# Performance work log

Hardware: AMD Instinct MI355X
Metric: run time of the kernel (lower is better)

Reference implementation:

```python
import jax, jax.numpy as jnp
import numpy as np

B, T, H, L = 64, 2048, 256, 16


def setup_inputs() -> dict:
    key = jax.random.key(0)
    ks = jax.random.split(key, 6)
    x = jax.random.normal(ks[0], (B, T, H), dtype=jnp.float32)
    tags = jax.random.randint(ks[1], (B, T), 0, L).astype(jnp.int32)
    mask = jnp.ones((B, T), dtype=bool)  # torchcrf requires mask[:,0] all on
    W = jax.random.normal(ks[2], (L, H), dtype=jnp.float32) * (1.0 / np.sqrt(H))
    b = jnp.zeros((L,), dtype=jnp.float32)
    # torchcrf initializes transitions ~ U(-0.1, 0.1)
    start_transitions = jax.random.uniform(ks[3], (L,), minval=-0.1, maxval=0.1)
    end_transitions = jax.random.uniform(ks[4], (L,), minval=-0.1, maxval=0.1)
    transitions = jax.random.uniform(ks[5], (L, L), minval=-0.1, maxval=0.1)
    return {"x": x, "W": W, "b": b,
            "start_transitions": start_transitions,
            "end_transitions": end_transitions,
            "transitions": transitions,
            "tags": tags, "mask": mask}


def reference(x, W, b, start_transitions, end_transitions, transitions, tags, mask):
    # Emitter: Linear(hidden_dim -> num_labels)
    emissions = jnp.einsum('bth,lh->btl', x, W) + b  # [B,T,L]
    maskf = mask.astype(emissions.dtype)             # [B,T]

    # ---- numerator: score of the gold tag path (vectorized, no scan) ----
    emit_gold = jnp.take_along_axis(emissions, tags[..., None].astype(jnp.int32), axis=2)[..., 0]  # [B,T]
    first_tags = tags[:, 0]
    score = start_transitions[first_tags] + emit_gold[:, 0]
    trans_gold = transitions[tags[:, :-1], tags[:, 1:]]  # [B,T-1]
    score = score + jnp.sum((trans_gold + emit_gold[:, 1:]) * maskf[:, 1:], axis=1)
    seq_ends = jnp.sum(mask.astype(jnp.int32), axis=1) - 1  # index of last valid step
    last_tags = jnp.take_along_axis(tags, seq_ends[:, None], axis=1)[:, 0]
    score = score + end_transitions[last_tags]

    # ---- denominator: forward algorithm (log partition) via lax.scan over time ----
    em_t = jnp.swapaxes(emissions, 0, 1)  # [T,B,L]
    mask_t = jnp.swapaxes(mask, 0, 1)     # [T,B]
    alpha0 = start_transitions[None, :] + em_t[0]  # [B,L]

    def step(alpha, inp):
        em, m = inp  # em: [B,L], m: [B]
        # logsumexp over previous label: alpha[b,i] + transitions[i,j] + em[b,j]
        nxt = jax.nn.logsumexp(alpha[:, :, None] + transitions[None, :, :] + em[:, None, :], axis=1)
        alpha = jnp.where(m[:, None], nxt, alpha)
        return alpha, None

    alphaT, _ = jax.lax.scan(step, alpha0, (em_t[1:], mask_t[1:]))
    denom = jax.nn.logsumexp(alphaT + end_transitions[None, :], axis=1)  # [B]

    llh = score - denom          # log-likelihood per sequence
    return -jnp.mean(llh)        # reduction='mean', nll = -crf(...)
```

## Files before the change

kernel.cpp:

```cpp
#include <hip/hip_runtime.h>
#include <math.h>


#define Bb 64
#define Tt 2048
#define Hh 256
#define Ll 16
#define CHUNK 32
#define NC (Tt / CHUNK)
#define ROWS 128
#define TSTR 20

typedef __attribute__((ext_vector_type(8))) short short8;
typedef __attribute__((ext_vector_type(4))) short short4v;
typedef __attribute__((ext_vector_type(4))) float f32x4;

__device__ __forceinline__ unsigned pk2bf(float a, float b) {
  unsigned ua = __float_as_uint(a) + 0x8000u;
  unsigned ub = __float_as_uint(b) + 0x8000u;
  return (ua >> 16) | (ub & 0xFFFF0000u);
}
__device__ __forceinline__ short8 pack8(float4 lo, float4 hi) {
  union { int4 i; short8 s; } u;
  u.i.x = pk2bf(lo.x, lo.y);
  u.i.y = pk2bf(lo.z, lo.w);
  u.i.z = pk2bf(hi.x, hi.y);
  u.i.w = pk2bf(hi.z, hi.w);
  return u.s;
}

#if __has_builtin(__builtin_amdgcn_mfma_f32_16x16x16bf16_1k)
#define MFMA16(a, b, c) __builtin_amdgcn_mfma_f32_16x16x16bf16_1k(a, b, c, 0, 0, 0)
#else
__device__ __forceinline__ f32x4 mfma16_asm(short4v a, short4v b, f32x4 c) {
  f32x4 d;
  asm("v_mfma_f32_16x16x16_bf16 %0, %1, %2, %3" : "=v"(d) : "v"(a), "v"(b), "v"(c));
  return d;
}
#define MFMA16(a, b, c) mfma16_asm(a, b, c)
#endif

__global__ __launch_bounds__(256, 4) void k_fused(const float* __restrict__ x,
                                                  const float* __restrict__ W,
                                                  const float* __restrict__ bias,
                                                  const float* __restrict__ strans,
                                                  const float* __restrict__ etrans,
                                                  const float* __restrict__ trans,
                                                  const int* __restrict__ tags,
                                                  float* __restrict__ em0,
                                                  float* __restrict__ Pout,
                                                  float* __restrict__ lscale,
                                                  float* __restrict__ score) {
  __shared__ float tile[ROWS * TSTR];
  __shared__ unsigned short ghb[ROWS * 16];
  __shared__ float Pbuf[4][16 * TSTR];

  const int tid = threadIdx.x, w = tid >> 6, lane = tid & 63;
  const int n = lane & 15, quad = lane >> 4;
  const int b = blockIdx.x >> 4, blk = blockIdx.x & 15;
  const int gc = blk * 4 + w;

  {
    const float4* wp4 = (const float4*)(W + (size_t)n * Hh) + quad * 2;
    float4 wr[16];
#pragma unroll
    for (int ks = 0; ks < 8; ++ks) { wr[2 * ks] = wp4[ks * 8]; wr[2 * ks + 1] = wp4[ks * 8 + 1]; }
    short8 Bf[8];
#pragma unroll
    for (int ks = 0; ks < 8; ++ks) Bf[ks] = pack8(wr[2 * ks], wr[2 * ks + 1]);
    float bs = bias[n];
    size_t Grow = (size_t)blockIdx.x * ROWS + w * 32 + n;
    const float4* xa = (const float4*)(x + Grow * Hh) + quad * 2;
    const float4* xb = (const float4*)(x + (Grow + 16) * Hh) + quad * 2;
    f32x4 acc0 = {0.f, 0.f, 0.f, 0.f}, acc1 = {0.f, 0.f, 0.f, 0.f};
    float4 ra[16];
#pragma unroll
    for (int ks = 0; ks < 8; ++ks) { ra[2 * ks] = xa[ks * 8]; ra[2 * ks + 1] = xa[ks * 8 + 1]; }
#pragma unroll
    for (int ks = 0; ks < 8; ++ks) {
      short8 a0 = pack8(ra[2 * ks], ra[2 * ks + 1]);
      acc0 = __builtin_amdgcn_mfma_f32_16x16x32_bf16(a0, Bf[ks], acc0, 0, 0, 0);
    }
#pragma unroll
    for (int ks = 0; ks < 8; ++ks) { ra[2 * ks] = xb[ks * 8]; ra[2 * ks + 1] = xb[ks * 8 + 1]; }
#pragma unroll
    for (int ks = 0; ks < 8; ++ks) {
      short8 a1 = pack8(ra[2 * ks], ra[2 * ks + 1]);
      acc1 = __builtin_amdgcn_mfma_f32_16x16x32_bf16(a1, Bf[ks], acc1, 0, 0, 0);
    }
#pragma unroll
    for (int r = 0; r < 4; ++r) {
      tile[(w * 32 + quad * 4 + r) * TSTR + n] = acc0[r] + bs;
      tile[(w * 32 + 16 + quad * 4 + r) * TSTR + n] = acc1[r] + bs;
    }
    if (blk == 0 && w == 0 && quad == 0) em0[b * 16 + n] = acc0[0] + bs;
  }
  __syncthreads();

  {
    float s2 = 0.f;
    if (lane < 32) {
      int rl = w * 32 + lane;
      int t = blk * ROWS + rl;
      int gt = b * Tt + t;
      int tag = tags[gt];
      float ev = tile[rl * TSTR + tag];
      if (t == 0) s2 = strans[tag] + ev;
      else        s2 = trans[tags[gt - 1] * 16 + tag] + ev;
      if (t == Tt - 1) s2 += etrans[tag];
    }
#pragma unroll
    for (int msk = 1; msk < 64; msk <<= 1) s2 += __shfl_xor(s2, msk);
    if (lane == 0) atomicAdd(score + b, s2);
  }

  float offsum = 0.f;
  {
    if (lane < 32) {
      int rl = w * 32 + lane;
      const float4* tp = (const float4*)(tile + rl * TSTR);
      float4 a0 = tp[0], a1 = tp[1], a2 = tp[2], a3 = tp[3];
      float m = fmaxf(fmaxf(fmaxf(fmaxf(a0.x, a0.y), fmaxf(a0.z, a0.w)),
                            fmaxf(fmaxf(a1.x, a1.y), fmaxf(a1.z, a1.w))),
                      fmaxf(fmaxf(fmaxf(a2.x, a2.y), fmaxf(a2.z, a2.w)),
                            fmaxf(fmaxf(a3.x, a3.y), fmaxf(a3.z, a3.w))));
      float4 e0 = make_float4(expf(a0.x - m), expf(a0.y - m), expf(a0.z - m), expf(a0.w - m));
      float4 e1 = make_float4(expf(a1.x - m), expf(a1.y - m), expf(a1.z - m), expf(a1.w - m));
      float4 e2 = make_float4(expf(a2.x - m), expf(a2.y - m), expf(a2.z - m), expf(a2.w - m));
      float4 e3 = make_float4(expf(a3.x - m), expf(a3.y - m), expf(a3.z - m), expf(a3.w - m));
      int4 lo, hi;
      lo.x = pk2bf(e0.x, e0.y); lo.y = pk2bf(e0.z, e0.w);
      lo.z = pk2bf(e1.x, e1.y); lo.w = pk2bf(e1.z, e1.w);
      hi.x = pk2bf(e2.x, e2.y); hi.y = pk2bf(e2.z, e2.w);
      hi.z = pk2bf(e3.x, e3.y); hi.w = pk2bf(e3.z, e3.w);
      ((int4*)ghb)[rl * 2] = lo;
      ((int4*)ghb)[rl * 2 + 1] = hi;
      int t = blk * ROWS + rl;
      offsum = (t >= 1) ? m : 0.f;
    }
#pragma unroll
    for (int msk = 1; msk < 64; msk <<= 1) offsum += __shfl_xor(offsum, msk);
  }
  __syncthreads();

  {
    union { unsigned u[2]; short4v s4; } ae;
    {
      float e0 = 0.25f * expf(trans[(quad * 4 + 0) * 16 + n]);
      float e1 = 0.25f * expf(trans[(quad * 4 + 1) * 16 + n]);
      float e2 = 0.25f * expf(trans[(quad * 4 + 2) * 16 + n]);
      float e3 = 0.25f * expf(trans[(quad * 4 + 3) * 16 + n]);
      ae.u[0] = pk2bf(e0, e1);
      ae.u[1] = pk2bf(e2, e3);
    }
    union { unsigned u[2]; short sh[4]; short4v s4; } bq;
    bq.u[0] = 0; bq.u[1] = 0;
    if ((n >> 2) == quad) bq.sh[n & 3] = (short)0x3F80;

    const int sbeg = (gc == 0) ? 1 : 0;
    const unsigned short* grow = ghb + (w * 32) * 16 + quad * 4;
    short4v Bq = bq.s4;
    f32x4 d;
#define PSTEP(ss) { \
      const unsigned* gp = (const unsigned*)(grow + (ss) * 16); \
      unsigned glo = gp[0], ghi = gp[1]; \
      f32x4 z = {0.f, 0.f, 0.f, 0.f}; \
      d = MFMA16(ae.s4, Bq, z); \
      d[0] *= __uint_as_float(glo << 16); \
      d[1] *= __uint_as_float(glo & 0xFFFF0000u); \
      d[2] *= __uint_as_float(ghi << 16); \
      d[3] *= __uint_as_float(ghi & 0xFFFF0000u); \
      union { unsigned pu[2]; short4v ps; } pb; \
      pb.pu[0] = pk2bf(d[0], d[1]); \
      pb.pu[1] = pk2bf(d[2], d[3]); \
      Bq = pb.ps; }
    if (sbeg == 0) PSTEP(0)
#pragma unroll
    for (int s = 1; s < CHUNK; ++s) PSTEP(s)
#undef PSTEP

    float mx = fmaxf(fmaxf(d[0], d[1]), fmaxf(d[2], d[3]));
#pragma unroll
    for (int msk = 1; msk < 64; msk <<= 1) mx = fmaxf(mx, __shfl_xor(mx, msk));
    float inv = __builtin_amdgcn_rcpf(mx);
    float off = offsum + (float)(CHUNK - sbeg) * 1.3862943611198906f + logf(mx);

    float* Pw = Pbuf[w];
#pragma unroll
    for (int r = 0; r < 4; ++r) Pw[n * TSTR + quad * 4 + r] = d[r] * inv;
    {
      int i = lane >> 2, jg = lane & 3;
      float4 pv = *(const float4*)(Pw + i * TSTR + jg * 4);
      ((float4*)(Pout + ((size_t)(b * NC + gc)) * 256))[lane] = pv;
      if (lane == 0) lscale[b * NC + gc] = off;
    }
  }
}

__global__ __launch_bounds__(256) void k_combine(const float* __restrict__ em0,
                                                 const float* __restrict__ P,
                                                 const float* __restrict__ lscale,
                                                 const float* __restrict__ strans,
                                                 const float* __restrict__ etrans,
                                                 float* __restrict__ denom) {
  int b = blockIdx.x, tid = threadIdx.x;
  __shared__ float Pl[NC * 256];
  const float4* src = (const float4*)(P + (size_t)b * NC * 256);
  float4* dst = (float4*)Pl;
  for (int idx = tid; idx < NC * 64; idx += 256) dst[idx] = src[idx];
  __syncthreads();
  if (tid >= 64) return;
  int lane = tid;
  float ls = lscale[b * NC + lane];
#pragma unroll
  for (int m = 1; m < 64; m <<= 1) ls += __shfl_xor(ls, m);

  int j = lane & 15, ig = lane >> 4;
  float a = strans[j] + em0[b * 16 + j];
  float m0 = a;
#pragma unroll
  for (int m = 1; m < 16; m <<= 1) m0 = fmaxf(m0, __shfl_xor(m0, m));
  float v = expf(a - m0);
  float o = m0 + ls;

  for (int cc = 0; cc < NC; ++cc) {
    const float* Pc = Pl + cc * 256;
    float part = 0.f;
#pragma unroll
    for (int r = 0; r < 4; ++r) {
      int srcl = (ig << 4) + ig * 4 + r;
      float vr = __shfl(v, srcl);
      part = fmaf(vr, Pc[(ig * 4 + r) * 16 + j], part);
    }
    part += __shfl_xor(part, 16);
    part += __shfl_xor(part, 32);
    if ((cc & 3) == 3) {
      float mx = part;
#pragma unroll
      for (int m = 1; m < 16; m <<= 1) mx = fmaxf(mx, __shfl_xor(mx, m));
      o += logf(mx);
      v = part * __builtin_amdgcn_rcpf(mx);
    } else {
      v = part;
    }
  }
  float sj = v * expf(etrans[j]);
#pragma unroll
  for (int m = 1; m < 16; m <<= 1) sj += __shfl_xor(sj, m);
  if (lane == 0) denom[b] = o + logf(sj);
}

__global__ __launch_bounds__(64) void k_final(const float* __restrict__ score,
                                              const float* __restrict__ denom,
                                              float* __restrict__ out) {
  int lane = threadIdx.x;
  float llh = score[lane] - denom[lane];
#pragma unroll
  for (int m = 1; m < 64; m <<= 1) llh += __shfl_xor(llh, m);
  if (lane == 0) out[0] = -llh * (1.0f / 64.0f);
}

extern "C" void kernel_launch(void* const* d_in, const int* in_sizes, int n_in,
                              void* d_out, int out_size, void* d_ws, size_t ws_size,
                              hipStream_t stream) {
  const float* x = (const float*)d_in[0];
  const float* W = (const float*)d_in[1];
  const float* bias = (const float*)d_in[2];
  const float* strans = (const float*)d_in[3];
  const float* etrans = (const float*)d_in[4];
  const float* trans = (const float*)d_in[5];
  const int* tags = (const int*)d_in[6];

  float* ws = (float*)d_ws;
  float* em0 = ws;
  float* P = em0 + Bb * 16;
  float* lscale = P + (size_t)Bb * NC * 256;
  float* score = lscale + Bb * NC;
  float* denom = score + Bb;
  float* out = (float*)d_out;

  hipMemsetAsync(score, 0, Bb * sizeof(float), stream);
  hipLaunchKernelGGL(k_fused, dim3(Bb * Tt / ROWS), dim3(256), 0, stream,
                     x, W, bias, strans, etrans, trans, tags, em0, P, lscale, score);
  hipLaunchKernelGGL(k_combine, dim3(Bb), dim3(256), 0, stream, em0, P, lscale, strans, etrans, denom);
  hipLaunchKernelGGL(k_final, dim3(1), dim3(64), 0, stream, score, denom, out);
}
```

Before: 241.2 us.

## Stage x through LDS with async double-buffered global_load_lds and per-wave scratch

```diff
diff --git a/kernel.cpp b/kernel.cpp
--- a/kernel.cpp
+++ b/kernel.cpp
@@ -39,6 +39,11 @@
 }
 #define MFMA16(a, b, c) mfma16_asm(a, b, c)
 #endif
+
+__device__ __forceinline__ void gload_lds16(const float* g, char* l) {
+  __builtin_amdgcn_global_load_lds((const __attribute__((address_space(1))) void*)g,
+                                   (__attribute__((address_space(3))) void*)l, 16, 0, 0);
+}
 
 __global__ __launch_bounds__(256, 4) void k_fused(const float* __restrict__ x,
                                                   const float* __restrict__ W,
@@ -51,60 +56,84 @@
                                                   float* __restrict__ Pout,
                                                   float* __restrict__ lscale,
                                                   float* __restrict__ score) {
-  __shared__ float tile[ROWS * TSTR];
-  __shared__ unsigned short ghb[ROWS * 16];
-  __shared__ float Pbuf[4][16 * TSTR];
+  __shared__ __align__(16) char smem[4 * 8192];
 
   const int tid = threadIdx.x, w = tid >> 6, lane = tid & 63;
   const int n = lane & 15, quad = lane >> 4;
   const int b = blockIdx.x >> 4, blk = blockIdx.x & 15;
   const int gc = blk * 4 + w;
-
+  char* xw = smem + w * 8192;
+
+  f32x4 acc0 = {0.f, 0.f, 0.f, 0.f}, acc1 = {0.f, 0.f, 0.f, 0.f};
+  float bs;
   {
     const float4* wp4 = (const float4*)(W + (size_t)n * Hh) + quad * 2;
-    float4 wr[16];
-#pragma unroll
-    for (int ks = 0; ks < 8; ++ks) { wr[2 * ks] = wp4[ks * 8]; wr[2 * ks + 1] = wp4[ks * 8 + 1]; }
+    float4 wv[16];
+#pragma unroll
+    for (int ks = 0; ks < 8; ++ks) { wv[2 * ks] = wp4[ks * 8]; wv[2 * ks + 1] = wp4[ks * 8 + 1]; }
+    bs = bias[n];
+
+    const size_t R0 = (size_t)blockIdx.x * ROWS + (size_t)w * 32;
+    const int gsel = (lane & 7) ^ ((lane >> 3) & 7);
+    const float* srcb = x + (R0 + (size_t)(lane >> 3)) * Hh + gsel * 4;
+
+#define STAGEI(cc, bb) { \
+      const float* sp_ = srcb + (cc) * 32; \
+      char* lb_ = xw + (bb) * 4096; \
+      gload_lds16(sp_,           lb_); \
+      gload_lds16(sp_ + 8 * Hh,  lb_ + 1024); \
+      gload_lds16(sp_ + 16 * Hh, lb_ + 2048); \
+      gload_lds16(sp_ + 24 * Hh, lb_ + 3072); }
+
+    STAGEI(0, 0)
+    STAGEI(1, 1)
+
     short8 Bf[8];
 #pragma unroll
-    for (int ks = 0; ks < 8; ++ks) Bf[ks] = pack8(wr[2 * ks], wr[2 * ks + 1]);
-    float bs = bias[n];
-    size_t Grow = (size_t)blockIdx.x * ROWS + w * 32 + n;
-    const float4* xa = (const float4*)(x + Grow * Hh) + quad * 2;
-    const float4* xb = (const float4*)(x + (Grow + 16) * Hh) + quad * 2;
-    f32x4 acc0 = {0.f, 0.f, 0.f, 0.f}, acc1 = {0.f, 0.f, 0.f, 0.f};
-    float4 ra[16];
-#pragma unroll
-    for (int ks = 0; ks < 8; ++ks) { ra[2 * ks] = xa[ks * 8]; ra[2 * ks + 1] = xa[ks * 8 + 1]; }
-#pragma unroll
-    for (int ks = 0; ks < 8; ++ks) {
-      short8 a0 = pack8(ra[2 * ks], ra[2 * ks + 1]);
-      acc0 = __builtin_amdgcn_mfma_f32_16x16x32_bf16(a0, Bf[ks], acc0, 0, 0, 0);
-    }
-#pragma unroll
-    for (int ks = 0; ks < 8; ++ks) { ra[2 * ks] = xb[ks * 8]; ra[2 * ks + 1] = xb[ks * 8 + 1]; }
-#pragma unroll
-    for (int ks = 0; ks < 8; ++ks) {
-      short8 a1 = pack8(ra[2 * ks], ra[2 * ks + 1]);
-      acc1 = __builtin_amdgcn_mfma_f32_16x16x32_bf16(a1, Bf[ks], acc1, 0, 0, 0);
-    }
+    for (int ks = 0; ks < 8; ++ks) Bf[ks] = pack8(wv[2 * ks], wv[2 * ks + 1]);
+
+    const int r7 = n & 7;
+    const unsigned o0 = (unsigned)(((2 * quad) ^ r7) << 4);
+    const unsigned o1 = (unsigned)(((2 * quad + 1) ^ r7) << 4);
+    const unsigned rowb = (unsigned)(n * 128);
+
+#pragma unroll
+    for (int c = 0; c < 8; ++c) {
+      if (c < 7) { asm volatile("s_waitcnt vmcnt(4)" ::: "memory"); }
+      else       { asm volatile("s_waitcnt vmcnt(0)" ::: "memory"); }
+      __builtin_amdgcn_sched_barrier(0);
+      const char* rb = xw + (c & 1) * 4096;
+      float4 v0 = *(const float4*)(rb + rowb + o0);
+      float4 v1 = *(const float4*)(rb + rowb + o1);
+      float4 u0 = *(const float4*)(rb + 2048 + rowb + o0);
+      float4 u1 = *(const float4*)(rb + 2048 + rowb + o1);
+      short8 a0 = pack8(v0, v1);
+      short8 a1 = pack8(u0, u1);
+      acc0 = __builtin_amdgcn_mfma_f32_16x16x32_bf16(a0, Bf[c], acc0, 0, 0, 0);
+      acc1 = __builtin_amdgcn_mfma_f32_16x16x32_bf16(a1, Bf[c], acc1, 0, 0, 0);
+      if (c + 2 < 8) STAGEI(c + 2, c & 1)
+    }
+#undef STAGEI
+  }
+
+  float* emw = (float*)xw;
+  {
 #pragma unroll
     for (int r = 0; r < 4; ++r) {
-      tile[(w * 32 + quad * 4 + r) * TSTR + n] = acc0[r] + bs;
-      tile[(w * 32 + 16 + quad * 4 + r) * TSTR + n] = acc1[r] + bs;
+      emw[(quad * 4 + r) * TSTR + n] = acc0[r] + bs;
+      emw[(16 + quad * 4 + r) * TSTR + n] = acc1[r] + bs;
     }
     if (blk == 0 && w == 0 && quad == 0) em0[b * 16 + n] = acc0[0] + bs;
   }
-  __syncthreads();
 
   {
     float s2 = 0.f;
     if (lane < 32) {
-      int rl = w * 32 + lane;
-      int t = blk * ROWS + rl;
+      int rl = lane;
+      int t = blk * ROWS + w * 32 + rl;
       int gt = b * Tt + t;
       int tag = tags[gt];
-      float ev = tile[rl * TSTR + tag];
+      float ev = emw[rl * TSTR + tag];
       if (t == 0) s2 = strans[tag] + ev;
       else        s2 = trans[tags[gt - 1] * 16 + tag] + ev;
       if (t == Tt - 1) s2 += etrans[tag];
@@ -114,11 +143,12 @@
     if (lane == 0) atomicAdd(score + b, s2);
   }
 
+  unsigned short* ghb = (unsigned short*)(xw + 2560);
   float offsum = 0.f;
   {
     if (lane < 32) {
-      int rl = w * 32 + lane;
-      const float4* tp = (const float4*)(tile + rl * TSTR);
+      int rl = lane;
+      const float4* tp = (const float4*)(emw + rl * TSTR);
       float4 a0 = tp[0], a1 = tp[1], a2 = tp[2], a3 = tp[3];
       float m = fmaxf(fmaxf(fmaxf(fmaxf(a0.x, a0.y), fmaxf(a0.z, a0.w)),
                             fmaxf(fmaxf(a1.x, a1.y), fmaxf(a1.z, a1.w))),
@@ -135,13 +165,12 @@
       hi.z = pk2bf(e3.x, e3.y); hi.w = pk2bf(e3.z, e3.w);
       ((int4*)ghb)[rl * 2] = lo;
       ((int4*)ghb)[rl * 2 + 1] = hi;
-      int t = blk * ROWS + rl;
+      int t = blk * ROWS + w * 32 + rl;
       offsum = (t >= 1) ? m : 0.f;
     }
 #pragma unroll
     for (int msk = 1; msk < 64; msk <<= 1) offsum += __shfl_xor(offsum, msk);
   }
-  __syncthreads();
 
   {
     union { unsigned u[2]; short4v s4; } ae;
@@ -158,7 +187,7 @@
     if ((n >> 2) == quad) bq.sh[n & 3] = (short)0x3F80;
 
     const int sbeg = (gc == 0) ? 1 : 0;
-    const unsigned short* grow = ghb + (w * 32) * 16 + quad * 4;
+    const unsigned short* grow = ghb + quad * 4;
     short4v Bq = bq.s4;
     f32x4 d;
 #define PSTEP(ss) { \
@@ -185,7 +214,7 @@
     float inv = __builtin_amdgcn_rcpf(mx);
     float off = offsum + (float)(CHUNK - sbeg) * 1.3862943611198906f + logf(mx);
 
-    float* Pw = Pbuf[w];
+    float* Pw = (float*)(xw + 3584);
 #pragma unroll
     for (int r = 0; r < 4; ++r) Pw[n * TSTR + quad * 4 + r] = d[r] * inv;
     {
```

Result: no change. 242.9 us (+0.7%).

## Split fused emission GEMM and chunk chain into separate kernels via global emissions

Applied to the files above, without the earlier changes.

```diff
diff --git a/kernel.cpp b/kernel.cpp
--- a/kernel.cpp
+++ b/kernel.cpp
@@ -8,7 +8,6 @@
 #define Ll 16
 #define CHUNK 32
 #define NC (Tt / CHUNK)
-#define ROWS 128
 #define TSTR 20
 
 typedef __attribute__((ext_vector_type(8))) short short8;
@@ -40,71 +39,99 @@
 #define MFMA16(a, b, c) mfma16_asm(a, b, c)
 #endif
 
-__global__ __launch_bounds__(256, 4) void k_fused(const float* __restrict__ x,
-                                                  const float* __restrict__ W,
-                                                  const float* __restrict__ bias,
+__global__ __launch_bounds__(256, 4) void k_emit(const float* __restrict__ x,
+                                                 const float* __restrict__ W,
+                                                 const float* __restrict__ bias,
+                                                 float* __restrict__ em) {
+  const int tid = threadIdx.x, w = tid >> 6, lane = tid & 63;
+  const int n = lane & 15, quad = lane >> 4;
+
+  short8 Bf[8];
+  {
+    const float* wbase = W + (size_t)n * Hh + quad * 8;
+#pragma unroll
+    for (int c = 0; c < 8; ++c) {
+      float4 w0 = *(const float4*)(wbase + c * 32);
+      float4 w1 = *(const float4*)(wbase + c * 32 + 4);
+      Bf[c] = pack8(w0, w1);
+    }
+  }
+  const float bs = bias[n];
+  const int wid = blockIdx.x * 4 + w;
+
+#pragma unroll
+  for (int s = 0; s < 2; ++s) {
+    const int mt = s * 4096 + wid;
+    const float* xb = x + (size_t)mt * 16 * Hh + (size_t)n * Hh + quad * 8;
+    float4 ra[16];
+#pragma unroll
+    for (int c = 0; c < 8; ++c) {
+      ra[2 * c] = *(const float4*)(xb + c * 32);
+      ra[2 * c + 1] = *(const float4*)(xb + c * 32 + 4);
+    }
+    f32x4 acc = {0.f, 0.f, 0.f, 0.f};
+#pragma unroll
+    for (int c = 0; c < 8; ++c) {
+      short8 a0 = pack8(ra[2 * c], ra[2 * c + 1]);
+      acc = __builtin_amdgcn_mfma_f32_16x16x32_bf16(a0, Bf[c], acc, 0, 0, 0);
+    }
+    float* eb = em + (size_t)mt * 256;
+#pragma unroll
+    for (int r = 0; r < 4; ++r) eb[(quad * 4 + r) * 16 + n] = acc[r] + bs;
+  }
+}
+
+__global__ __launch_bounds__(256, 4) void k_chain(const float* __restrict__ em,
                                                   const float* __restrict__ strans,
                                                   const float* __restrict__ etrans,
                                                   const float* __restrict__ trans,
                                                   const int* __restrict__ tags,
-                                                  float* __restrict__ em0,
                                                   float* __restrict__ Pout,
                                                   float* __restrict__ lscale,
                                                   float* __restrict__ score) {
-  __shared__ float tile[ROWS * TSTR];
-  __shared__ unsigned short ghb[ROWS * 16];
-  __shared__ float Pbuf[4][16 * TSTR];
+  __shared__ float emL[4][CHUNK * 16];
+  __shared__ unsigned short ghbS[4][CHUNK * 16];
+  __shared__ float PbufS[4][16 * TSTR];
 
   const int tid = threadIdx.x, w = tid >> 6, lane = tid & 63;
   const int n = lane & 15, quad = lane >> 4;
-  const int b = blockIdx.x >> 4, blk = blockIdx.x & 15;
-  const int gc = blk * 4 + w;
-
-  {
-    const float4* wp4 = (const float4*)(W + (size_t)n * Hh) + quad * 2;
-    float4 wr[16];
-#pragma unroll
-    for (int ks = 0; ks < 8; ++ks) { wr[2 * ks] = wp4[ks * 8]; wr[2 * ks + 1] = wp4[ks * 8 + 1]; }
-    short8 Bf[8];
-#pragma unroll
-    for (int ks = 0; ks < 8; ++ks) Bf[ks] = pack8(wr[2 * ks], wr[2 * ks + 1]);
-    float bs = bias[n];
-    size_t Grow = (size_t)blockIdx.x * ROWS + w * 32 + n;
-    const float4* xa = (const float4*)(x + Grow * Hh) + quad * 2;
-    const float4* xb = (const float4*)(x + (Grow + 16) * Hh) + quad * 2;
-    f32x4 acc0 = {0.f, 0.f, 0.f, 0.f}, acc1 = {0.f, 0.f, 0.f, 0.f};
-    float4 ra[16];
-#pragma unroll
-    for (int ks = 0; ks < 8; ++ks) { ra[2 * ks] = xa[ks * 8]; ra[2 * ks + 1] = xa[ks * 8 + 1]; }
-#pragma unroll
-    for (int ks = 0; ks < 8; ++ks) {
-      short8 a0 = pack8(ra[2 * ks], ra[2 * ks + 1]);
-      acc0 = __builtin_amdgcn_mfma_f32_16x16x32_bf16(a0, Bf[ks], acc0, 0, 0, 0);
-    }
-#pragma unroll
-    for (int ks = 0; ks < 8; ++ks) { ra[2 * ks] = xb[ks * 8]; ra[2 * ks + 1] = xb[ks * 8 + 1]; }
-#pragma unroll
-    for (int ks = 0; ks < 8; ++ks) {
-      short8 a1 = pack8(ra[2 * ks], ra[2 * ks + 1]);
-      acc1 = __builtin_amdgcn_mfma_f32_16x16x32_bf16(a1, Bf[ks], acc1, 0, 0, 0);
-    }
-#pragma unroll
-    for (int r = 0; r < 4; ++r) {
-      tile[(w * 32 + quad * 4 + r) * TSTR + n] = acc0[r] + bs;
-      tile[(w * 32 + 16 + quad * 4 + r) * TSTR + n] = acc1[r] + bs;
-    }
-    if (blk == 0 && w == 0 && quad == 0) em0[b * 16 + n] = acc0[0] + bs;
-  }
-  __syncthreads();
+  const int C = blockIdx.x * 4 + w;
+  const int b = C >> 6, gc = C & 63;
+
+  float* emw = emL[w];
+  unsigned short* ghb = ghbS[w];
+
+  const float4* eb = (const float4*)(em + (size_t)C * (CHUNK * 16));
+  float4 v0 = eb[lane * 2], v1 = eb[lane * 2 + 1];
+  ((float4*)emw)[lane * 2] = v0;
+  ((float4*)emw)[lane * 2 + 1] = v1;
+
+  float offsum;
+  {
+    float m = fmaxf(fmaxf(fmaxf(v0.x, v0.y), fmaxf(v0.z, v0.w)),
+                    fmaxf(fmaxf(v1.x, v1.y), fmaxf(v1.z, v1.w)));
+    m = fmaxf(m, __shfl_xor(m, 1));
+    float e0 = expf(v0.x - m), e1 = expf(v0.y - m), e2 = expf(v0.z - m), e3 = expf(v0.w - m);
+    float e4 = expf(v1.x - m), e5 = expf(v1.y - m), e6 = expf(v1.z - m), e7 = expf(v1.w - m);
+    int4 pk;
+    pk.x = pk2bf(e0, e1); pk.y = pk2bf(e2, e3);
+    pk.z = pk2bf(e4, e5); pk.w = pk2bf(e6, e7);
+    ((int4*)ghb)[lane] = pk;
+    int t = gc * CHUNK + (lane >> 1);
+    float ov = (((lane & 1) == 0) && (t >= 1)) ? m : 0.f;
+#pragma unroll
+    for (int msk = 1; msk < 64; msk <<= 1) ov += __shfl_xor(ov, msk);
+    offsum = ov;
+  }
 
   {
     float s2 = 0.f;
     if (lane < 32) {
-      int rl = w * 32 + lane;
-      int t = blk * ROWS + rl;
+      int rl = lane;
+      int t = gc * CHUNK + rl;
       int gt = b * Tt + t;
       int tag = tags[gt];
-      float ev = tile[rl * TSTR + tag];
+      float ev = emw[rl * 16 + tag];
       if (t == 0) s2 = strans[tag] + ev;
       else        s2 = trans[tags[gt - 1] * 16 + tag] + ev;
       if (t == Tt - 1) s2 += etrans[tag];
@@ -113,35 +140,6 @@
     for (int msk = 1; msk < 64; msk <<= 1) s2 += __shfl_xor(s2, msk);
     if (lane == 0) atomicAdd(score + b, s2);
   }
-
-  float offsum = 0.f;
-  {
-    if (lane < 32) {
-      int rl = w * 32 + lane;
-      const float4* tp = (const float4*)(tile + rl * TSTR);
-      float4 a0 = tp[0], a1 = tp[1], a2 = tp[2], a3 = tp[3];
-      float m = fmaxf(fmaxf(fmaxf(fmaxf(a0.x, a0.y), fmaxf(a0.z, a0.w)),
-                            fmaxf(fmaxf(a1.x, a1.y), fmaxf(a1.z, a1.w))),
-                      fmaxf(fmaxf(fmaxf(a2.x, a2.y), fmaxf(a2.z, a2.w)),
-                            fmaxf(fmaxf(a3.x, a3.y), fmaxf(a3.z, a3.w))));
-      float4 e0 = make_float4(expf(a0.x - m), expf(a0.y - m), expf(a0.z - m), expf(a0.w - m));
-      float4 e1 = make_float4(expf(a1.x - m), expf(a1.y - m), expf(a1.z - m), expf(a1.w - m));
-      float4 e2 = make_float4(expf(a2.x - m), expf(a2.y - m), expf(a2.z - m), expf(a2.w - m));
-      float4 e3 = make_float4(expf(a3.x - m), expf(a3.y - m), expf(a3.z - m), expf(a3.w - m));
-      int4 lo, hi;
-      lo.x = pk2bf(e0.x, e0.y); lo.y = pk2bf(e0.z, e0.w);
-      lo.z = pk2bf(e1.x, e1.y); lo.w = pk2bf(e1.z, e1.w);
-      hi.x = pk2bf(e2.x, e2.y); hi.y = pk2bf(e2.z, e2.w);
-      hi.z = pk2bf(e3.x, e3.y); hi.w = pk2bf(e3.z, e3.w);
-      ((int4*)ghb)[rl * 2] = lo;
-      ((int4*)ghb)[rl * 2 + 1] = hi;
-      int t = blk * ROWS + rl;
-      offsum = (t >= 1) ? m : 0.f;
-    }
-#pragma unroll
-    for (int msk = 1; msk < 64; msk <<= 1) offsum += __shfl_xor(offsum, msk);
-  }
-  __syncthreads();
 
   {
     union { unsigned u[2]; short4v s4; } ae;
@@ -158,7 +156,7 @@
     if ((n >> 2) == quad) bq.sh[n & 3] = (short)0x3F80;
 
     const int sbeg = (gc == 0) ? 1 : 0;
-    const unsigned short* grow = ghb + (w * 32) * 16 + quad * 4;
+    const unsigned short* grow = ghb + quad * 4;
     short4v Bq = bq.s4;
     f32x4 d;
 #define PSTEP(ss) { \
@@ -185,19 +183,19 @@
     float inv = __builtin_amdgcn_rcpf(mx);
     float off = offsum + (float)(CHUNK - sbeg) * 1.3862943611198906f + logf(mx);
 
-    float* Pw = Pbuf[w];
+    float* Pw = PbufS[w];
 #pragma unroll
     for (int r = 0; r < 4; ++r) Pw[n * TSTR + quad * 4 + r] = d[r] * inv;
     {
       int i = lane >> 2, jg = lane & 3;
       float4 pv = *(const float4*)(Pw + i * TSTR + jg * 4);
-      ((float4*)(Pout + ((size_t)(b * NC + gc)) * 256))[lane] = pv;
-      if (lane == 0) lscale[b * NC + gc] = off;
-    }
-  }
-}
-
-__global__ __launch_bounds__(256) void k_combine(const float* __restrict__ em0,
+      ((float4*)(Pout + ((size_t)C) * 256))[lane] = pv;
+      if (lane == 0) lscale[C] = off;
+    }
+  }
+}
+
+__global__ __launch_bounds__(256) void k_combine(const float* __restrict__ em,
                                                  const float* __restrict__ P,
                                                  const float* __restrict__ lscale,
                                                  const float* __restrict__ strans,
@@ -216,7 +214,7 @@
   for (int m = 1; m < 64; m <<= 1) ls += __shfl_xor(ls, m);
 
   int j = lane & 15, ig = lane >> 4;
-  float a = strans[j] + em0[b * 16 + j];
+  float a = strans[j] + em[(size_t)b * (Tt * 16) + j];
   float m0 = a;
 #pragma unroll
   for (int m = 1; m < 16; m <<= 1) m0 = fmaxf(m0, __shfl_xor(m0, m));
@@ -272,16 +270,17 @@
   const int* tags = (const int*)d_in[6];
 
   float* ws = (float*)d_ws;
-  float* em0 = ws;
-  float* P = em0 + Bb * 16;
+  float* em = ws;
+  float* P = em + (size_t)Bb * Tt * 16;
   float* lscale = P + (size_t)Bb * NC * 256;
   float* score = lscale + Bb * NC;
   float* denom = score + Bb;
   float* out = (float*)d_out;
 
   hipMemsetAsync(score, 0, Bb * sizeof(float), stream);
-  hipLaunchKernelGGL(k_fused, dim3(Bb * Tt / ROWS), dim3(256), 0, stream,
-                     x, W, bias, strans, etrans, trans, tags, em0, P, lscale, score);
-  hipLaunchKernelGGL(k_combine, dim3(Bb), dim3(256), 0, stream, em0, P, lscale, strans, etrans, denom);
+  hipLaunchKernelGGL(k_emit, dim3(1024), dim3(256), 0, stream, x, W, bias, em);
+  hipLaunchKernelGGL(k_chain, dim3(1024), dim3(256), 0, stream,
+                     em, strans, etrans, trans, tags, P, lscale, score);
+  hipLaunchKernelGGL(k_combine, dim3(Bb), dim3(256), 0, stream, em, P, lscale, strans, etrans, denom);
   hipLaunchKernelGGL(k_final, dim3(1), dim3(64), 0, stream, score, denom, out);
 }
```

Result: slower. 261.8 us (+8.5%).
